# Optimization experiments

Hardware: AMD Instinct MI355X
Metric: run time of the kernel (lower is better)

Reference implementation:

```python
import jax, jax.numpy as jnp
import numpy as np

D_MODEL = 1024
N_HEADS = 16
HEAD_DIM = D_MODEL // N_HEADS
WINDOW = 128  # radius w; attend to [i-w, i+w]


def setup_inputs() -> dict:
    key = jax.random.key(0)
    ks = jax.random.split(key, 5)
    scale = 1.0 / np.sqrt(D_MODEL)
    x = jax.random.normal(ks[0], (2, 2048, D_MODEL), dtype=jnp.float32)
    # nn.MultiheadAttention packed projections
    in_proj_w = jax.random.normal(ks[1], (3 * D_MODEL, D_MODEL), dtype=jnp.float32) * scale
    in_proj_b = jnp.zeros((3 * D_MODEL,), dtype=jnp.float32)
    out_w = jax.random.normal(ks[2], (D_MODEL, D_MODEL), dtype=jnp.float32) * scale
    out_b = jnp.zeros((D_MODEL,), dtype=jnp.float32)
    return {"x": x, "in_proj_w": in_proj_w, "in_proj_b": in_proj_b,
            "out_w": out_w, "out_b": out_b}


def reference(x, in_proj_w, in_proj_b, out_w, out_b):
    B, S, D = x.shape
    H, Dh = N_HEADS, HEAD_DIM
    # packed qkv projection (PyTorch: x @ W^T + b)
    qkv = x @ in_proj_w.T + in_proj_b              # [B, S, 3D]
    q, k, v = jnp.split(qkv, 3, axis=-1)
    q = q.reshape(B, S, H, Dh)
    k = k.reshape(B, S, H, Dh)
    v = v.reshape(B, S, H, Dh)
    scores = jnp.einsum('bqhd,bkhd->bhqk', q, k) / np.sqrt(Dh)  # [B,H,S,S]
    # window mask: allowed iff |i - j| <= WINDOW
    idx = jnp.arange(S)
    allowed = jnp.abs(idx[:, None] - idx[None, :]) <= WINDOW    # [S, S]
    scores = jnp.where(allowed[None, None], scores, -jnp.inf)
    attn = jax.nn.softmax(scores, axis=-1)
    out = jnp.einsum('bhqk,bkhd->bqhd', attn, v).reshape(B, S, D)
    return out @ out_w.T + out_b
```

## Files before the change

kernel.cpp:

```cpp
#include <hip/hip_runtime.h>
#include <hip/hip_bf16.h>


#define S_LEN 2048
#define NH 16
#define DH 64
#define DM 1024
#define WIN 128
#define K_DIM 1024

typedef __attribute__((ext_vector_type(8))) short short8;
typedef __attribute__((ext_vector_type(4))) short short4_t;
typedef __attribute__((ext_vector_type(4))) float f32x4;
typedef __attribute__((ext_vector_type(16))) float f32x16;

__device__ __forceinline__ unsigned short f2bf(float f){
  unsigned u = __float_as_uint(f);
  u += 0x7fffu + ((u >> 16) & 1u);
  return (unsigned short)(u >> 16);
}
__device__ __forceinline__ unsigned pk2(float lo, float hi){
  __hip_bfloat162 h = __float22bfloat162_rn(float2{lo, hi});
  return *reinterpret_cast<unsigned*>(&h);
}
__device__ __forceinline__ void async16(void* l, const void* g){
  __builtin_amdgcn_global_load_lds((const __attribute__((address_space(1))) void*)g,
                                   (__attribute__((address_space(3))) void*)l, 16, 0, 0);
}

__global__ void cvt_all(const float* __restrict__ x, const float* __restrict__ w1,
                        const float* __restrict__ wo,
                        short* __restrict__ xb, short* __restrict__ w1b,
                        short* __restrict__ wob){
  int b = blockIdx.x;
  const float* src; short* dst; int base;
  if (b < 4096)      { src = x;  dst = xb;  base = b; }
  else if (b < 7168) { src = w1; dst = w1b; base = b - 4096; }
  else               { src = wo; dst = wob; base = b - 7168; }
  int i = (base * 256 + threadIdx.x) * 4;
  float4 v = *(const float4*)(src + i);
  short4_t o;
  o.x = (short)f2bf(v.x); o.y = (short)f2bf(v.y);
  o.z = (short)f2bf(v.z); o.w = (short)f2bf(v.w);
  *(short4_t*)(dst + i) = o;
}

__global__ __launch_bounds__(256) void gemm_qkv(
    const short* __restrict__ A, const short* __restrict__ Bw,
    const float* __restrict__ bias,
    short* __restrict__ Qb, short* __restrict__ Kb, short* __restrict__ Vb)
{
  __shared__ short As[128*32], Bs[128*32];
  int tid = threadIdx.x;
  int lane = tid & 63, wv = tid >> 6;
  int wr = wv >> 1, wc = wv & 1;
  int lr = lane & 15, lh = lane >> 4;
  int m0 = blockIdx.y * 128, n0 = blockIdx.x * 128;

  f32x4 acc[4][4] = {};
  for (int kt = 0; kt < K_DIM; kt += 32) {
    #pragma unroll
    for (int i = 0; i < 2; ++i) {
      int c = i*256 + tid;
      int row = c >> 2, col = (c & 3) << 3;
      async16(&As[c*8], A  + (size_t)(m0+row)*K_DIM + kt + col);
      async16(&Bs[c*8], Bw + (size_t)(n0+row)*K_DIM + kt + col);
    }
    __syncthreads();
    short8 af[4], bfr[4];
    #pragma unroll
    for (int m = 0; m < 4; ++m) af[m]  = *(const short8*)&As[(wr*64 + m*16 + lr)*32 + lh*8];
    #pragma unroll
    for (int n = 0; n < 4; ++n) bfr[n] = *(const short8*)&Bs[(wc*64 + n*16 + lr)*32 + lh*8];
    #pragma unroll
    for (int m = 0; m < 4; ++m)
      #pragma unroll
      for (int n = 0; n < 4; ++n)
        acc[m][n] = __builtin_amdgcn_mfma_f32_16x16x32_bf16(af[m], bfr[n], acc[m][n], 0, 0, 0);
    __syncthreads();
  }
  #pragma unroll
  for (int m = 0; m < 4; ++m) {
    #pragma unroll
    for (int n = 0; n < 4; ++n) {
      int col = n0 + wc*64 + n*16 + lr;
      float bv = bias[col];
      int which = col >> 10, cc = col & 1023;
      int h = cc >> 6, d = cc & 63;
      float scl = which == 0 ? 0.125f : 1.0f;
      #pragma unroll
      for (int r = 0; r < 4; ++r) {
        int grow = m0 + wr*64 + m*16 + lh*4 + r;
        int b = grow >> 11, s = grow & 2047;
        float v = (acc[m][n][r] + bv) * scl;
        if (which == 2) {
          Vb[((size_t)(b*NH + h)*DH + d)*S_LEN + s] = (short)f2bf(v);
        } else {
          short* dst = which == 0 ? Qb : Kb;
          dst[(((size_t)b*NH + h)*S_LEN + s)*DH + d] = (short)f2bf(v);
        }
      }
    }
  }
}

__global__ __launch_bounds__(512) void gemm_out(
    const short* __restrict__ A, const short* __restrict__ Bw,
    const float* __restrict__ bias, float* __restrict__ Out)
{
  __shared__ short As[128*32], Bs[128*32];
  int tid = threadIdx.x;
  int lane = tid & 63, wv = tid >> 6;
  int wr = wv >> 2, wc = wv & 3;
  int lr = lane & 15, lh = lane >> 4;
  int m0 = blockIdx.y * 128, n0 = blockIdx.x * 128;

  f32x4 acc[4][2] = {};
  for (int kt = 0; kt < K_DIM; kt += 32) {
    int row = tid >> 2, col = (tid & 3) << 3;
    async16(&As[tid*8], A  + (size_t)(m0+row)*K_DIM + kt + col);
    async16(&Bs[tid*8], Bw + (size_t)(n0+row)*K_DIM + kt + col);
    __syncthreads();
    short8 af[4], bfr[2];
    #pragma unroll
    for (int m = 0; m < 4; ++m) af[m]  = *(const short8*)&As[(wr*64 + m*16 + lr)*32 + lh*8];
    #pragma unroll
    for (int n = 0; n < 2; ++n) bfr[n] = *(const short8*)&Bs[(wc*32 + n*16 + lr)*32 + lh*8];
    #pragma unroll
    for (int m = 0; m < 4; ++m)
      #pragma unroll
      for (int n = 0; n < 2; ++n)
        acc[m][n] = __builtin_amdgcn_mfma_f32_16x16x32_bf16(af[m], bfr[n], acc[m][n], 0, 0, 0);
    __syncthreads();
  }
  #pragma unroll
  for (int m = 0; m < 4; ++m) {
    #pragma unroll
    for (int n = 0; n < 2; ++n) {
      int col = n0 + wc*32 + n*16 + lr;
      float bv = bias[col];
      #pragma unroll
      for (int r = 0; r < 4; ++r) {
        int grow = m0 + wr*64 + m*16 + lh*4 + r;
        Out[(size_t)grow*DM + col] = acc[m][n][r] + bv;
      }
    }
  }
}

__global__ __launch_bounds__(256) void attn_mfma(
    const short* __restrict__ Qb, const short* __restrict__ Kb,
    const short* __restrict__ VTb, short* __restrict__ Ob)
{
  int tid = threadIdx.x;
  int lane = tid & 63, wv = tid >> 6;
  int q31 = lane & 31, h2 = lane >> 5;
  int bh = blockIdx.y;
  int q0w = blockIdx.x * 128 + wv * 32;
  int qa = q0w + q31;

  const short* Qg = Qb  + (size_t)bh * S_LEN * DH;
  const short* Kg = Kb  + (size_t)bh * S_LEN * DH;
  const short* Vg = VTb + (size_t)bh * DH * S_LEN;

  short8 qf[4];
  #pragma unroll
  for (int kc = 0; kc < 4; ++kc)
    qf[kc] = *(const short8*)(Qg + (size_t)qa * DH + kc*16 + h2*8);

  int ks = q0w - WIN; if (ks < 0) ks = 0;
  int ke = q0w + 32 + WIN; if (ke > S_LEN) ke = S_LEN;

  f32x16 o0 = {}, o1 = {};
  float m = -1e37f, l = 0.f;

  for (int t0 = ks; t0 < ke; t0 += 32) {
    f32x16 s = {};
    #pragma unroll
    for (int kc = 0; kc < 4; ++kc) {
      short8 kf = *(const short8*)(Kg + (size_t)(t0 + q31) * DH + kc*16 + h2*8);
      s = __builtin_amdgcn_mfma_f32_32x32x16_bf16(kf, qf[kc], s, 0, 0, 0);
    }
    float p[16];
    float tm = -1e38f;
    #pragma unroll
    for (int r = 0; r < 16; ++r) {
      int key = t0 + (r & 3) + 8*(r >> 2) + 4*h2;
      bool ok = (key >= qa - WIN) && (key <= qa + WIN);
      p[r] = ok ? s[r] : -1e38f;
      tm = fmaxf(tm, p[r]);
    }
    tm = fmaxf(tm, __shfl_xor(tm, 32, 64));
    float mn = fmaxf(m, tm);
    float sc = __expf(m - mn);
    float ts = 0.f;
    #pragma unroll
    for (int r = 0; r < 16; ++r) { p[r] = __expf(p[r] - mn); ts += p[r]; }
    ts += __shfl_xor(ts, 32, 64);
    l = l * sc + ts;
    m = mn;
    #pragma unroll
    for (int r = 0; r < 16; ++r) { o0[r] *= sc; o1[r] *= sc; }

    #pragma unroll
    for (int kc2 = 0; kc2 < 2; ++kc2) {
      unsigned A1 = pk2(p[kc2*8+0], p[kc2*8+1]);
      unsigned A2 = pk2(p[kc2*8+2], p[kc2*8+3]);
      unsigned B1 = pk2(p[kc2*8+4], p[kc2*8+5]);
      unsigned B2 = pk2(p[kc2*8+6], p[kc2*8+7]);
      unsigned sA1 = (unsigned)__shfl_xor((int)A1, 32, 64);
      unsigned sA2 = (unsigned)__shfl_xor((int)A2, 32, 64);
      unsigned sB1 = (unsigned)__shfl_xor((int)B1, 32, 64);
      unsigned sB2 = (unsigned)__shfl_xor((int)B2, 32, 64);
      union { unsigned u[4]; short8 v; } pa;
      pa.u[0] = h2 ? sB1 : A1;
      pa.u[1] = h2 ? sB2 : A2;
      pa.u[2] = h2 ? B1 : sA1;
      pa.u[3] = h2 ? B2 : sA2;
      #pragma unroll
      for (int mt = 0; mt < 2; ++mt) {
        short8 vf = *(const short8*)(Vg + (size_t)(mt*32 + q31) * S_LEN + t0 + kc2*16 + h2*8);
        if (mt == 0) o0 = __builtin_amdgcn_mfma_f32_32x32x16_bf16(vf, pa.v, o0, 0, 0, 0);
        else         o1 = __builtin_amdgcn_mfma_f32_32x32x16_bf16(vf, pa.v, o1, 0, 0, 0);
      }
    }
  }

  float inv = 1.0f / l;
  int b = bh >> 4, hh = bh & 15;
  unsigned* Orow = (unsigned*)Ob + ((size_t)b*S_LEN + qa) * (DM/2) + hh*32;
  #pragma unroll
  for (int mt = 0; mt < 2; ++mt) {
    #pragma unroll
    for (int aa = 0; aa < 4; ++aa) {
      #pragma unroll
      for (int e = 0; e < 2; ++e) {
        int r = 4*aa + 2*e;
        float x0 = (mt ? o1[r]   : o0[r])   * inv;
        float x1 = (mt ? o1[r+1] : o0[r+1]) * inv;
        int d = 2*e + 8*aa + 4*h2 + 32*mt;
        Orow[d >> 1] = pk2(x0, x1);
      }
    }
  }
}

extern "C" void kernel_launch(void* const* d_in, const int* in_sizes, int n_in,
                              void* d_out, int out_size, void* d_ws, size_t ws_size,
                              hipStream_t stream) {
  const float* x  = (const float*)d_in[0];
  const float* w1 = (const float*)d_in[1];
  const float* b1 = (const float*)d_in[2];
  const float* wo = (const float*)d_in[3];
  const float* bo = (const float*)d_in[4];
  float* out = (float*)d_out;

  char* ws = (char*)d_ws;
  short* xb  = (short*)(ws);
  short* w1b = (short*)(ws + (size_t)8*1024*1024);
  short* wob = (short*)(ws + (size_t)14*1024*1024);
  short* Qb  = (short*)(ws + (size_t)16*1024*1024);
  short* Kb  = (short*)(ws + (size_t)24*1024*1024);
  short* VTb = (short*)(ws + (size_t)32*1024*1024);
  short* Ab  = (short*)(ws + (size_t)40*1024*1024);

  cvt_all<<<dim3(8192), dim3(256), 0, stream>>>(x, w1, wo, xb, w1b, wob);
  gemm_qkv<<<dim3(24, 32), dim3(256), 0, stream>>>(xb, w1b, b1, Qb, Kb, VTb);
  attn_mfma<<<dim3(16, 32), dim3(256), 0, stream>>>(Qb, Kb, VTb, Ab);
  gemm_out<<<dim3(8, 32), dim3(512), 0, stream>>>(Ab, wob, bo, out);
}
```

Baseline: 170.3 us.

## Double K-tile depth with XOR-swizzled LDS and vectorize V stores in GEMMs

Both projection GEMMs now stage a K-tile of 64 instead of 32 per iteration. This halves the number of barrier pairs and issues more MFMAs between syncs. Shared-memory tiles use an XOR swizzle of 16-byte chunks by row to cut LDS bank conflicts on fragment reads. The QKV epilogue writes the transposed V output as a 4-element short vector rather than scalar stores. LDS use doubles, which could lower occupancy.

```diff
diff --git a/kernel.cpp b/kernel.cpp
--- a/kernel.cpp
+++ b/kernel.cpp
@@ -50,7 +50,7 @@
     const float* __restrict__ bias,
     short* __restrict__ Qb, short* __restrict__ Kb, short* __restrict__ Vb)
 {
-  __shared__ short As[128*32], Bs[128*32];
+  __shared__ short As[128*64], Bs[128*64];
   int tid = threadIdx.x;
   int lane = tid & 63, wv = tid >> 6;
   int wr = wv >> 1, wc = wv & 1;
@@ -58,25 +58,34 @@
   int m0 = blockIdx.y * 128, n0 = blockIdx.x * 128;
 
   f32x4 acc[4][4] = {};
-  for (int kt = 0; kt < K_DIM; kt += 32) {
-    #pragma unroll
-    for (int i = 0; i < 2; ++i) {
-      int c = i*256 + tid;
-      int row = c >> 2, col = (c & 3) << 3;
-      async16(&As[c*8], A  + (size_t)(m0+row)*K_DIM + kt + col);
-      async16(&Bs[c*8], Bw + (size_t)(n0+row)*K_DIM + kt + col);
-    }
-    __syncthreads();
-    short8 af[4], bfr[4];
-    #pragma unroll
-    for (int m = 0; m < 4; ++m) af[m]  = *(const short8*)&As[(wr*64 + m*16 + lr)*32 + lh*8];
-    #pragma unroll
-    for (int n = 0; n < 4; ++n) bfr[n] = *(const short8*)&Bs[(wc*64 + n*16 + lr)*32 + lh*8];
+  for (int kt = 0; kt < K_DIM; kt += 64) {
+    #pragma unroll
+    for (int j = 0; j < 4; ++j) {
+      int off = j*256 + tid;
+      int lrow = off >> 3, slin = off & 7;
+      int sg = slin ^ (lrow & 7);
+      async16(&As[lrow*64 + slin*8], A  + (size_t)(m0+lrow)*K_DIM + kt + sg*8);
+      async16(&Bs[lrow*64 + slin*8], Bw + (size_t)(n0+lrow)*K_DIM + kt + sg*8);
+    }
+    __syncthreads();
+    short8 af[4][2], bfr[4][2];
+    #pragma unroll
+    for (int m = 0; m < 4; ++m)
+      #pragma unroll
+      for (int kk = 0; kk < 2; ++kk)
+        af[m][kk]  = *(const short8*)&As[(wr*64 + m*16 + lr)*64 + (((kk*4 + lh) ^ (lr & 7))*8)];
+    #pragma unroll
+    for (int n = 0; n < 4; ++n)
+      #pragma unroll
+      for (int kk = 0; kk < 2; ++kk)
+        bfr[n][kk] = *(const short8*)&Bs[(wc*64 + n*16 + lr)*64 + (((kk*4 + lh) ^ (lr & 7))*8)];
     #pragma unroll
     for (int m = 0; m < 4; ++m)
       #pragma unroll
       for (int n = 0; n < 4; ++n)
-        acc[m][n] = __builtin_amdgcn_mfma_f32_16x16x32_bf16(af[m], bfr[n], acc[m][n], 0, 0, 0);
+        #pragma unroll
+        for (int kk = 0; kk < 2; ++kk)
+          acc[m][n] = __builtin_amdgcn_mfma_f32_16x16x32_bf16(af[m][kk], bfr[n][kk], acc[m][n], 0, 0, 0);
     __syncthreads();
   }
   #pragma unroll
@@ -88,16 +97,21 @@
       int which = col >> 10, cc = col & 1023;
       int h = cc >> 6, d = cc & 63;
       float scl = which == 0 ? 0.125f : 1.0f;
-      #pragma unroll
-      for (int r = 0; r < 4; ++r) {
-        int grow = m0 + wr*64 + m*16 + lh*4 + r;
-        int b = grow >> 11, s = grow & 2047;
-        float v = (acc[m][n][r] + bv) * scl;
-        if (which == 2) {
-          Vb[((size_t)(b*NH + h)*DH + d)*S_LEN + s] = (short)f2bf(v);
-        } else {
-          short* dst = which == 0 ? Qb : Kb;
-          dst[(((size_t)b*NH + h)*S_LEN + s)*DH + d] = (short)f2bf(v);
+      int growb = m0 + wr*64 + m*16 + lh*4;
+      int b = growb >> 11, s0 = growb & 2047;
+      if (which == 2) {
+        short4_t vv;
+        vv.x = (short)f2bf(acc[m][n][0] + bv);
+        vv.y = (short)f2bf(acc[m][n][1] + bv);
+        vv.z = (short)f2bf(acc[m][n][2] + bv);
+        vv.w = (short)f2bf(acc[m][n][3] + bv);
+        *(short4_t*)&Vb[((size_t)(b*NH + h)*DH + d)*S_LEN + s0] = vv;
+      } else {
+        short* dst = which == 0 ? Qb : Kb;
+        #pragma unroll
+        for (int r = 0; r < 4; ++r) {
+          float v = (acc[m][n][r] + bv) * scl;
+          dst[(((size_t)b*NH + h)*S_LEN + s0 + r)*DH + d] = (short)f2bf(v);
         }
       }
     }
@@ -108,7 +122,7 @@
     const short* __restrict__ A, const short* __restrict__ Bw,
     const float* __restrict__ bias, float* __restrict__ Out)
 {
-  __shared__ short As[128*32], Bs[128*32];
+  __shared__ short As[128*64], Bs[128*64];
   int tid = threadIdx.x;
   int lane = tid & 63, wv = tid >> 6;
   int wr = wv >> 2, wc = wv & 3;
@@ -116,21 +130,34 @@
   int m0 = blockIdx.y * 128, n0 = blockIdx.x * 128;
 
   f32x4 acc[4][2] = {};
-  for (int kt = 0; kt < K_DIM; kt += 32) {
-    int row = tid >> 2, col = (tid & 3) << 3;
-    async16(&As[tid*8], A  + (size_t)(m0+row)*K_DIM + kt + col);
-    async16(&Bs[tid*8], Bw + (size_t)(n0+row)*K_DIM + kt + col);
-    __syncthreads();
-    short8 af[4], bfr[2];
-    #pragma unroll
-    for (int m = 0; m < 4; ++m) af[m]  = *(const short8*)&As[(wr*64 + m*16 + lr)*32 + lh*8];
-    #pragma unroll
-    for (int n = 0; n < 2; ++n) bfr[n] = *(const short8*)&Bs[(wc*32 + n*16 + lr)*32 + lh*8];
+  for (int kt = 0; kt < K_DIM; kt += 64) {
+    #pragma unroll
+    for (int j = 0; j < 2; ++j) {
+      int off = j*512 + tid;
+      int lrow = off >> 3, slin = off & 7;
+      int sg = slin ^ (lrow & 7);
+      async16(&As[lrow*64 + slin*8], A  + (size_t)(m0+lrow)*K_DIM + kt + sg*8);
+      async16(&Bs[lrow*64 + slin*8], Bw + (size_t)(n0+lrow)*K_DIM + kt + sg*8);
+    }
+    __syncthreads();
+    short8 af[4][2], bfr[2][2];
+    #pragma unroll
+    for (int m = 0; m < 4; ++m)
+      #pragma unroll
+      for (int kk = 0; kk < 2; ++kk)
+        af[m][kk]  = *(const short8*)&As[(wr*64 + m*16 + lr)*64 + (((kk*4 + lh) ^ (lr & 7))*8)];
+    #pragma unroll
+    for (int n = 0; n < 2; ++n)
+      #pragma unroll
+      for (int kk = 0; kk < 2; ++kk)
+        bfr[n][kk] = *(const short8*)&Bs[(wc*32 + n*16 + lr)*64 + (((kk*4 + lh) ^ (lr & 7))*8)];
     #pragma unroll
     for (int m = 0; m < 4; ++m)
       #pragma unroll
       for (int n = 0; n < 2; ++n)
-        acc[m][n] = __builtin_amdgcn_mfma_f32_16x16x32_bf16(af[m], bfr[n], acc[m][n], 0, 0, 0);
+        #pragma unroll
+        for (int kk = 0; kk < 2; ++kk)
+          acc[m][n] = __builtin_amdgcn_mfma_f32_16x16x32_bf16(af[m][kk], bfr[n][kk], acc[m][n], 0, 0, 0);
     __syncthreads();
   }
   #pragma unroll
```

Measured after the change: 171.3 us. No clear change (+0.6%).
